# Optimization experiments

Measured on AMD Instinct MI355X. Metric: run time of the kernel, lower is better.

Reference implementation:

```python
import jax, jax.numpy as jnp
import numpy as np

STEPS = 10          # points in t_grid -> STEPS-1 RK4 intervals
TRACE_STEPS = 2     # Hutchinson probes per dynamics eval
T_FINAL = 1.0
CLAMP = 100.0


def odefun(t, z, W1, b1, tw1, W2, b2):
    # time-conditioned 2-layer tanh MLP (canonical FFJORD dynamics)
    h = jnp.tanh(z @ W1 + b1 + t * tw1)
    return h @ W2 + b2


def setup_inputs() -> dict:
    key = jax.random.key(0)
    B, D, H = 2048, 512, 1024
    ks = jax.random.split(key, 4)
    s1 = 1.0 / np.sqrt(D)
    s2 = 1.0 / np.sqrt(H)
    return {
        "x": jax.random.normal(ks[0], (B, D), jnp.float32),
        "W1": jax.random.normal(ks[1], (D, H), jnp.float32) * s1,
        "b1": jnp.zeros((H,), jnp.float32),
        "tw1": jax.random.normal(ks[2], (H,), jnp.float32) * 0.1,
        "W2": jax.random.normal(ks[3], (H, D), jnp.float32) * s2,
        "b2": jnp.zeros((D,), jnp.float32),
    }


def reference(x, W1, b1, tw1, W2, b2):
    params = (W1, b1, tw1, W2, b2)
    B, D = x.shape

    def divergence_estimate(t, z, e):
        # torch detaches z before the grad call -> stop_gradient here
        z_sg = jax.lax.stop_gradient(z)
        f, vjp_fn = jax.vjp(lambda zz: odefun(t, zz, *params), z_sg)
        etf = vjp_fn(e)[0]                      # e^T J  (Hutchinson probe)
        return f, jnp.sum(etf * e, axis=-1)     # [B]

    def augmented_dynamics(t, state, key):
        z = state[:, :-1]                        # [B, D]
        div_est = jnp.zeros((B,), state.dtype)
        f_z = None
        for i in range(TRACE_STEPS):             # small fixed loop
            e = jax.random.randint(jax.random.fold_in(key, i), z.shape, 0, 2).astype(z.dtype) * 2.0 - 1.0
            f_z, div = divergence_estimate(t, z, e)
            div_est = div_est + div
        div_est = jnp.clip(div_est / TRACE_STEPS, -CLAMP, CLAMP)
        return jnp.concatenate([f_z, -div_est[:, None]], axis=-1)

    t_grid = jnp.linspace(0.0, T_FINAL, STEPS)
    state0 = jnp.concatenate([x, jnp.zeros((B, 1), x.dtype)], axis=-1)  # [B, D+1]

    def step(carry, t01):
        state, key = carry
        t0, t1 = t01[0], t01[1]
        dt = t1 - t0
        key, k1k, k2k, k3k, k4k = jax.random.split(key, 5)
        # torchdiffeq 'rk4' = Kutta's 3/8-rule variant (rk4_alt_step_func)
        k1 = augmented_dynamics(t0, state, k1k)
        k2 = augmented_dynamics(t0 + dt / 3.0, state + dt * k1 / 3.0, k2k)
        k3 = augmented_dynamics(t0 + dt * 2.0 / 3.0, state + dt * (k2 - k1 / 3.0), k3k)
        k4 = augmented_dynamics(t1, state + dt * (k1 - k2 + k3), k4k)
        state = state + (k1 + 3.0 * (k2 + k3) + k4) * dt * 0.125
        return (state, key), None

    t_pairs = jnp.stack([t_grid[:-1], t_grid[1:]], axis=-1)  # [STEPS-1, 2]
    (state, _), _ = jax.lax.scan(step, (state0, jax.random.key(1234)), t_pairs)

    rep, probsolve = state[:, :-1], state[:, -1]
    logprob = -0.5 * jnp.sum(rep * rep, axis=-1) + probsolve
    return rep, logprob
```

## Files before the change

kernel.cpp:

```cpp
#include <hip/hip_runtime.h>
#include <stdint.h>


#define B_N 2048
#define D_N 512
#define H_N 1024
#define BD (B_N * D_N)

typedef unsigned short u16;
typedef __attribute__((ext_vector_type(8))) short s16x8;
typedef __attribute__((ext_vector_type(4))) float f32x4;

typedef __attribute__((address_space(1))) const uint32_t ga_u32;
typedef __attribute__((address_space(3))) uint32_t ls_u32;

#if __has_builtin(__builtin_amdgcn_alignbit)
#define ROTL32(x, r) __builtin_amdgcn_alignbit((x), (x), 32 - (r))
#else
#define ROTL32(x, r) (((x) << (r)) | ((x) >> (32 - (r))))
#endif

__device__ __forceinline__ u16 f2bf(float f) {
  union { float f; uint32_t u; } c; c.f = f;
  uint32_t r = c.u + 0x7FFFu + ((c.u >> 16) & 1u);
  return (u16)(r >> 16);
}

struct U2 { uint32_t x, y; };

__device__ __forceinline__ U2 tf2x32(uint32_t k0, uint32_t k1, uint32_t x0, uint32_t x1) {
  uint32_t k2 = k0 ^ k1 ^ 0x1BD11BDAu;
#define RND(r) { x0 += x1; x1 = ROTL32(x1, r); x1 ^= x0; }
  x0 += k0; x1 += k1;
  RND(13) RND(15) RND(26) RND(6)
  x0 += k1; x1 += k2 + 1u;
  RND(17) RND(29) RND(16) RND(24)
  x0 += k2; x1 += k0 + 2u;
  RND(13) RND(15) RND(26) RND(6)
  x0 += k0; x1 += k1 + 3u;
  RND(17) RND(29) RND(16) RND(24)
  x0 += k1; x1 += k2 + 4u;
  RND(13) RND(15) RND(26) RND(6)
  x0 += k2; x1 += k0 + 5u;
#undef RND
  U2 r; r.x = x0; r.y = x1; return r;
}

__device__ __forceinline__ void keysched_body(uint32_t* ekeys) {
  uint32_t kx = 0u, ky = 1234u;
  for (int s = 0; s < 9; ++s) {
    for (int st = 0; st < 4; ++st) {
      U2 kst = tf2x32(kx, ky, 0u, (uint32_t)(st + 1));
      for (int pr = 0; pr < 2; ++pr) {
        U2 fo = tf2x32(kst.x, kst.y, 0u, (uint32_t)pr);
        U2 k2 = tf2x32(fo.x, fo.y, 0u, 1u);
        ekeys[(s * 4 + st) * 4 + pr * 2 + 0] = k2.x;
        ekeys[(s * 4 + st) * 4 + pr * 2 + 1] = k2.y;
      }
    }
    U2 c = tf2x32(kx, ky, 0u, 0u);
    kx = c.x; ky = c.y;
  }
}

__device__ __forceinline__ void egen_item(int t2, u16* __restrict__ ebf,
                                          const uint32_t* __restrict__ keys) {
  int stage = t2 >> 16, rem = t2 & 65535;
  int probe = rem >> 15, idx = rem & 32767;
  uint32_t p0 = (uint32_t)idx * 32;
  uint32_t k0 = keys[stage * 4 + probe * 2], k1 = keys[stage * 4 + probe * 2 + 1];
  uint4* dst = (uint4*)(ebf + (size_t)stage * (2 * (size_t)BD) + (size_t)probe * BD + (size_t)idx * 32);
#pragma unroll
  for (int g = 0; g < 4; ++g) {
    uint32_t pr[4];
#pragma unroll
    for (int h = 0; h < 4; ++h) {
      uint32_t c0 = p0 + g * 8 + h * 2;
      U2 r0 = tf2x32(k0, k1, 0u, c0);
      U2 r1 = tf2x32(k0, k1, 0u, c0 + 1u);
      pr[h] = (((r0.x ^ r0.y) & 1u) ? 0x3F80u : 0xBF80u) |
              (((r1.x ^ r1.y) & 1u) ? 0x3F800000u : 0xBF800000u);
    }
    uint4 v; v.x = pr[0]; v.y = pr[1]; v.z = pr[2]; v.w = pr[3];
    dst[g] = v;
  }
}

__device__ __forceinline__ void f1_tile(u16* S, int tile,
    const u16* __restrict__ zin, const u16* __restrict__ e0g, const u16* __restrict__ e1g,
    const u16* __restrict__ W1T, const u16* __restrict__ W2b,
    const float* __restrict__ b1v, const float* __restrict__ tw1v, float tstage,
    u16* __restrict__ hbuf, float* __restrict__ div0, float* __restrict__ div1) {
  const int tid = threadIdx.x, wave = tid >> 6, lane = tid & 63;
  const int bm = tile >> 4, bh = tile & 15;
  const int row0 = bm * 64, col0 = bh * 64;
  const int wm = wave >> 1, wn = wave & 1, r16 = lane & 15, q = lane >> 4;
  const int srow = lane >> 2, scol = (lane & 3) * 8;

  f32x4 az[2][2], au0[2][2], au1[2][2], av0[2][2], av1[2][2];
#pragma unroll
  for (int i = 0; i < 2; ++i)
#pragma unroll
    for (int j = 0; j < 2; ++j) {
      az[i][j] = (f32x4){0,0,0,0}; au0[i][j] = (f32x4){0,0,0,0}; au1[i][j] = (f32x4){0,0,0,0};
      av0[i][j] = (f32x4){0,0,0,0}; av1[i][j] = (f32x4){0,0,0,0};
    }

  const size_t arow = (size_t)(row0 + wave * 16 + srow) * 512 + scol;
  const size_t brow = (size_t)(col0 + wave * 16 + srow) * 512 + scol;
  auto stage = [&](int kt, int buf) {
    u16* b = S + buf * 10240;
    __builtin_amdgcn_global_load_lds((ga_u32*)(zin + arow + kt), (ls_u32*)(b + 0    + wave * 512), 16, 0, 0);
    __builtin_amdgcn_global_load_lds((ga_u32*)(e0g + arow + kt), (ls_u32*)(b + 2048 + wave * 512), 16, 0, 0);
    __builtin_amdgcn_global_load_lds((ga_u32*)(e1g + arow + kt), (ls_u32*)(b + 4096 + wave * 512), 16, 0, 0);
    __builtin_amdgcn_global_load_lds((ga_u32*)(W1T + brow + kt), (ls_u32*)(b + 6144 + wave * 512), 16, 0, 0);
    __builtin_amdgcn_global_load_lds((ga_u32*)(W2b + brow + kt), (ls_u32*)(b + 8192 + wave * 512), 16, 0, 0);
  };
  stage(0, 0);
  for (int it = 0; it < 16; ++it) {
    const int buf = it & 1;
    __syncthreads();
    if (it + 1 < 16) stage((it + 1) * 32, buf ^ 1);
    const u16* b = S + buf * 10240;
    s16x8 zf[2], e0f[2], e1f[2], w1f[2], w2f[2];
#pragma unroll
    for (int i = 0; i < 2; ++i) {
      const int ao = (wm * 32 + i * 16 + r16) * 32 + q * 8;
      zf[i]  = *(const s16x8*)(b + 0    + ao);
      e0f[i] = *(const s16x8*)(b + 2048 + ao);
      e1f[i] = *(const s16x8*)(b + 4096 + ao);
    }
#pragma unroll
    for (int j = 0; j < 2; ++j) {
      const int bo = (wn * 32 + j * 16 + r16) * 32 + q * 8;
      w1f[j] = *(const s16x8*)(b + 6144 + bo);
      w2f[j] = *(const s16x8*)(b + 8192 + bo);
    }
#pragma unroll
    for (int i = 0; i < 2; ++i)
#pragma unroll
      for (int j = 0; j < 2; ++j) {
        az[i][j]  = __builtin_amdgcn_mfma_f32_16x16x32_bf16(zf[i],  w1f[j], az[i][j],  0, 0, 0);
        au0[i][j] = __builtin_amdgcn_mfma_f32_16x16x32_bf16(e0f[i], w1f[j], au0[i][j], 0, 0, 0);
        au1[i][j] = __builtin_amdgcn_mfma_f32_16x16x32_bf16(e1f[i], w1f[j], au1[i][j], 0, 0, 0);
        av0[i][j] = __builtin_amdgcn_mfma_f32_16x16x32_bf16(e0f[i], w2f[j], av0[i][j], 0, 0, 0);
        av1[i][j] = __builtin_amdgcn_mfma_f32_16x16x32_bf16(e1f[i], w2f[j], av1[i][j], 0, 0, 0);
      }
  }

  float d0s[2][4], d1s[2][4];
#pragma unroll
  for (int i = 0; i < 2; ++i)
#pragma unroll
    for (int r = 0; r < 4; ++r) { d0s[i][r] = 0.f; d1s[i][r] = 0.f; }

#pragma unroll
  for (int j = 0; j < 2; ++j) {
    const int gcol = col0 + wn * 32 + j * 16 + r16;
    const float colb = b1v[gcol] + tstage * tw1v[gcol];
#pragma unroll
    for (int i = 0; i < 2; ++i) {
      const int rbase = row0 + wm * 32 + i * 16 + q * 4;
#pragma unroll
      for (int r = 0; r < 4; ++r) {
        float hv = tanhf(az[i][j][r] + colb);
        hbuf[(size_t)(rbase + r) * H_N + gcol] = f2bf(hv);
        float s = 1.f - hv * hv;
        d0s[i][r] += s * au0[i][j][r] * av0[i][j][r];
        d1s[i][r] += s * au1[i][j][r] * av1[i][j][r];
      }
    }
  }
#pragma unroll
  for (int i = 0; i < 2; ++i)
#pragma unroll
    for (int r = 0; r < 4; ++r) {
      float a = d0s[i][r], bb = d1s[i][r];
#pragma unroll
      for (int m = 1; m < 16; m <<= 1) { a += __shfl_xor(a, m); bb += __shfl_xor(bb, m); }
      if (r16 == 0) {
        int grow = row0 + wm * 32 + i * 16 + q * 4 + r;
        atomicAdd(&div0[grow], a);
        atomicAdd(&div1[grow], bb);
      }
    }
}

__device__ __forceinline__ void f3_tile(u16* S, int tile,
    const u16* __restrict__ hbuf, const u16* __restrict__ W2T, const float* __restrict__ b2v,
    float* __restrict__ z, float* __restrict__ ACC, float* __restrict__ T,
    u16* __restrict__ zin, float dt, int st,
    float* __restrict__ lp, float* __restrict__ div0, float* __restrict__ div1, float wdt) {
  const int tid = threadIdx.x, wave = tid >> 6, lane = tid & 63;
  const int bm = tile >> 4, bn = tile & 15;
  const int row0 = bm * 64, col0 = bn * 32;
  const int r16 = lane & 15, q = lane >> 4;
  const int srow = lane >> 2, scol = (lane & 3) * 8;

  if (bn == 0 && tid < 64) {
    int b = row0 + tid;
    float c = 0.5f * (div0[b] + div1[b]);
    c = fminf(fmaxf(c, -100.f), 100.f);
    lp[b] -= wdt * c;
    div0[b] = 0.f; div1[b] = 0.f;
  }

  f32x4 acc[2];
  acc[0] = (f32x4){0,0,0,0}; acc[1] = (f32x4){0,0,0,0};

  const size_t arow = (size_t)(row0 + wave * 16 + srow) * 1024 + scol;
  const size_t brow = (size_t)(col0 + (wave & 1) * 16 + srow) * 1024 + scol;
  auto stage = [&](int kt, int buf) {
    u16* b = S + buf * 10240;
    __builtin_amdgcn_global_load_lds((ga_u32*)(hbuf + arow + kt), (ls_u32*)(b + wave * 512), 16, 0, 0);
    if (wave < 2)
      __builtin_amdgcn_global_load_lds((ga_u32*)(W2T + brow + kt), (ls_u32*)(b + 2048 + wave * 512), 16, 0, 0);
  };
  stage(0, 0);
  for (int it = 0; it < 32; ++it) {
    const int buf = it & 1;
    __syncthreads();
    if (it + 1 < 32) stage((it + 1) * 32, buf ^ 1);
    const u16* b = S + buf * 10240;
    s16x8 af  = *(const s16x8*)(b + (wave * 16 + r16) * 32 + q * 8);
    s16x8 bf0 = *(const s16x8*)(b + 2048 + r16 * 32 + q * 8);
    s16x8 bf1 = *(const s16x8*)(b + 2048 + (16 + r16) * 32 + q * 8);
    acc[0] = __builtin_amdgcn_mfma_f32_16x16x32_bf16(af, bf0, acc[0], 0, 0, 0);
    acc[1] = __builtin_amdgcn_mfma_f32_16x16x32_bf16(af, bf1, acc[1], 0, 0, 0);
  }

#pragma unroll
  for (int j = 0; j < 2; ++j) {
    const int gcol = col0 + j * 16 + r16;
    const float cb = b2v[gcol];
    const int rbase = row0 + wave * 16 + q * 4;
#pragma unroll
    for (int r = 0; r < 4; ++r) {
      const size_t idx = (size_t)(rbase + r) * D_N + gcol;
      const float f = acc[j][r] + cb;
      if (st == 0) {
        ACC[idx] = dt * 0.125f * f;
        T[idx]   = dt * f;
        zin[idx] = f2bf(z[idx] + dt * f * (1.f / 3.f));
      } else if (st == 1) {
        float t_ = T[idx];
        ACC[idx] += 0.375f * dt * f;
        zin[idx] = f2bf(z[idx] + dt * f - t_ * (1.f / 3.f));
        T[idx]   = t_ - dt * f;
      } else if (st == 2) {
        ACC[idx] += 0.375f * dt * f;
        zin[idx] = f2bf(z[idx] + T[idx] + dt * f);
      } else {
        float zn = z[idx] + ACC[idx] + dt * 0.125f * f;
        z[idx]   = zn;
        zin[idx] = f2bf(zn);
      }
    }
  }
}

__device__ __forceinline__ void bar_sync(uint32_t* cnt, uint32_t target) {
  __syncthreads();
  __threadfence();
  if (threadIdx.x == 0) {
    __hip_atomic_fetch_add(cnt, 1u, __ATOMIC_RELAXED, __HIP_MEMORY_SCOPE_AGENT);
    uint32_t v = __hip_atomic_load(cnt, __ATOMIC_RELAXED, __HIP_MEMORY_SCOPE_AGENT);
    while (v < target) {
      __builtin_amdgcn_s_sleep(2);
      v = __hip_atomic_load(cnt, __ATOMIC_RELAXED, __HIP_MEMORY_SCOPE_AGENT);
    }
  }
  __syncthreads();
  __threadfence();
}

__global__ __launch_bounds__(256, 2)
void k_main(const float* __restrict__ x, const float* __restrict__ W1,
            const float* __restrict__ b1v, const float* __restrict__ tw1v,
            const float* __restrict__ W2, const float* __restrict__ b2v,
            float* __restrict__ out, uint32_t* __restrict__ keys, u16* __restrict__ ebf,
            float* __restrict__ z, float* __restrict__ ACC, float* __restrict__ T,
            u16* __restrict__ zin, u16* __restrict__ hbuf,
            u16* __restrict__ W1T, u16* __restrict__ W2b, u16* __restrict__ W2T,
            float* __restrict__ lp, float* __restrict__ div0, float* __restrict__ div1,
            uint32_t* __restrict__ bar) {
  __shared__ u16 S[2 * 10240];
  const int gtid = blockIdx.x * 256 + threadIdx.x;
  const int gsz = gridDim.x * 256;
  const int slab = blockIdx.x >> 4;
  const int li   = blockIdx.x & 15;
  uint32_t* scnt = bar + slab * 32;
  uint32_t* gcnt = bar + 32 * 32;

  if (gtid == 0) keysched_body(keys);
  for (int i = gtid; i < BD; i += gsz) { float v = x[i]; z[i] = v; zin[i] = f2bf(v); }
  for (int i = gtid; i < B_N; i += gsz) { lp[i] = 0.f; div0[i] = 0.f; div1[i] = 0.f; }
  for (int i = gtid; i < D_N * H_N; i += gsz) {
    int c = i / D_N, r = i - c * D_N;
    W1T[i] = f2bf(W1[(size_t)r * H_N + c]);
  }
  for (int i = gtid; i < H_N * D_N; i += gsz) W2b[i] = f2bf(W2[i]);
  for (int i = gtid; i < H_N * D_N; i += gsz) {
    int c = i / H_N, r = i - c * H_N;
    W2T[i] = f2bf(W2[(size_t)r * D_N + c]);
  }
  bar_sync(gcnt, 512);

  for (int t2 = gtid; t2 < 36 * 65536; t2 += gsz) egen_item(t2, ebf, keys);
  bar_sync(gcnt, 1024);

  uint32_t tgt = 16;
  for (int sg = 0; sg < 36; ++sg) {
    const int s = sg >> 2, st = sg & 3;
    const float t0 = (float)s / 9.0f, t1 = (float)(s + 1) / 9.0f, dt = t1 - t0;
    const float tst = (st == 0) ? t0 : (st == 1) ? (t0 + dt / 3.0f)
                   : (st == 2) ? (t0 + dt * 2.0f / 3.0f) : t1;
    const float wdt = dt * 0.125f * ((st == 1 || st == 2) ? 3.0f : 1.0f);
    const u16* e0g = ebf + (size_t)sg * (2 * (size_t)BD);
    const u16* e1g = e0g + BD;
    f1_tile(S, slab * 16 + li, zin, e0g, e1g, W1T, W2b, b1v, tw1v, tst, hbuf, div0, div1);
    bar_sync(scnt, tgt); tgt += 16;
    f3_tile(S, slab * 16 + li, hbuf, W2T, b2v, z, ACC, T, zin, dt, st, lp, div0, div1, wdt);
    bar_sync(scnt, tgt); tgt += 16;
  }

  {
    const int wave = threadIdx.x >> 6, lane = threadIdx.x & 63;
    int b = slab * 64 + li * 4 + wave;
    const float* zr = z + (size_t)b * D_N;
    float ss = 0.f;
    for (int d = lane; d < D_N; d += 64) {
      float v = zr[d];
      out[(size_t)b * D_N + d] = v;
      ss += v * v;
    }
    for (int off = 32; off; off >>= 1) ss += __shfl_down(ss, off);
    if (lane == 0) out[BD + b] = -0.5f * ss + lp[b];
  }
}

__global__ void k_keysched(uint32_t* __restrict__ ekeys) {
  if (threadIdx.x == 0 && blockIdx.x == 0) keysched_body(ekeys);
}
__global__ void kegen_g(u16* __restrict__ ebf, const uint32_t* __restrict__ keys) {
  int t = blockIdx.x * 256 + threadIdx.x;
  if (t < 36 * 65536) egen_item(t, ebf, keys);
}
__global__ void k_init(const float* __restrict__ x, float* __restrict__ z, u16* __restrict__ zin,
                       float* __restrict__ lp, float* __restrict__ d0, float* __restrict__ d1) {
  int i = blockIdx.x * 256 + threadIdx.x;
  if (i < BD) { float v = x[i]; z[i] = v; zin[i] = f2bf(v); }
  if (i < B_N) { lp[i] = 0.f; d0[i] = 0.f; d1[i] = 0.f; }
}
__global__ void k_cvtT(const float* __restrict__ src, u16* __restrict__ dst, int R, int C) {
  int i = blockIdx.x * 256 + threadIdx.x;
  if (i >= R * C) return;
  int c = i / R, r = i - c * R;
  dst[i] = f2bf(src[(size_t)r * C + c]);
}
__global__ void k_cvt(const float* __restrict__ src, u16* __restrict__ dst, int n) {
  int i = blockIdx.x * 256 + threadIdx.x;
  if (i < n) dst[i] = f2bf(src[i]);
}
__global__ void k_sentinel(float* __restrict__ out, int n) {
  int i = blockIdx.x * 256 + threadIdx.x;
  if (i < n) out[i] = 12345.0f;
}
__global__ __launch_bounds__(256) void kf1_g(
    const u16* zin, const u16* e0g, const u16* e1g, const u16* W1T, const u16* W2b,
    const float* b1v, const float* tw1v, float tstage,
    u16* hbuf, float* div0, float* div1) {
  __shared__ u16 S[2 * 10240];
  f1_tile(S, blockIdx.x, zin, e0g, e1g, W1T, W2b, b1v, tw1v, tstage, hbuf, div0, div1);
}
__global__ __launch_bounds__(256) void kf3_g(
    const u16* hbuf, const u16* W2T, const float* b2v,
    float* z, float* ACC, float* T, u16* zin, float dt, int st,
    float* lp, float* div0, float* div1, float wdt) {
  __shared__ u16 S[2 * 10240];
  f3_tile(S, blockIdx.x, hbuf, W2T, b2v, z, ACC, T, zin, dt, st, lp, div0, div1, wdt);
}
__global__ void k_out(const float* __restrict__ z, const float* __restrict__ lp,
                      float* __restrict__ out) {
  int b = blockIdx.x, t = threadIdx.x;
  const float* zr = z + (size_t)b * D_N;
  float ss = 0.f;
  for (int d = t; d < D_N; d += 256) {
    float v = zr[d];
    out[(size_t)b * D_N + d] = v;
    ss += v * v;
  }
  for (int off = 32; off > 0; off >>= 1) ss += __shfl_down(ss, off);
  __shared__ float red[4];
  if ((t & 63) == 0) red[t >> 6] = ss;
  __syncthreads();
  if (t == 0) out[(size_t)BD + b] = -0.5f * (red[0] + red[1] + red[2] + red[3]) + lp[b];
}

extern "C" void kernel_launch(void* const* d_in, const int* in_sizes, int n_in,
                              void* d_out, int out_size, void* d_ws, size_t ws_size,
                              hipStream_t stream) {
  const float* x   = (const float*)d_in[0];
  const float* W1  = (const float*)d_in[1];
  const float* b1  = (const float*)d_in[2];
  const float* tw1 = (const float*)d_in[3];
  const float* W2  = (const float*)d_in[4];
  const float* b2  = (const float*)d_in[5];
  float* outp = (float*)d_out;

  const size_t NEEDED = (size_t)180 << 20;
  if (ws_size < NEEDED) {
    k_sentinel<<<(BD + B_N + 255) / 256, 256, 0, stream>>>(outp, BD + B_N);
    return;
  }
  char* w = (char*)d_ws;
  auto carve = [&](size_t bytes) { char* p = w; w += (bytes + 255) & ~(size_t)255; return p; };
  uint32_t* bar  = (uint32_t*)carve(33 * 32 * sizeof(uint32_t));
  uint32_t* keys = (uint32_t*)carve(144 * sizeof(uint32_t));
  u16* ebf   = (u16*)carve((size_t)36 * 2 * BD * 2);
  float* z   = (float*)carve((size_t)BD * 4);
  float* ACC = (float*)carve((size_t)BD * 4);
  float* T   = (float*)carve((size_t)BD * 4);
  u16* zin   = (u16*)carve((size_t)BD * 2);
  u16* hbuf  = (u16*)carve((size_t)B_N * H_N * 2);
  u16* W1T   = (u16*)carve((size_t)H_N * D_N * 2);
  u16* W2b   = (u16*)carve((size_t)H_N * D_N * 2);
  u16* W2T   = (u16*)carve((size_t)D_N * H_N * 2);
  float* lp   = (float*)carve((size_t)B_N * 4);
  float* div0 = (float*)carve((size_t)B_N * 4);
  float* div1 = (float*)carve((size_t)B_N * 4);

  int maxb = 0;
  hipError_t orc = hipOccupancyMaxActiveBlocksPerMultiprocessor(&maxb, (const void*)k_main, 256, 0);
  if (orc == hipSuccess && maxb >= 2) {
    hipMemsetAsync(bar, 0, 33 * 32 * sizeof(uint32_t), stream);
    void* params[] = { (void*)&x, (void*)&W1, (void*)&b1, (void*)&tw1, (void*)&W2, (void*)&b2,
                       (void*)&outp, (void*)&keys, (void*)&ebf, (void*)&z, (void*)&ACC, (void*)&T,
                       (void*)&zin, (void*)&hbuf, (void*)&W1T, (void*)&W2b, (void*)&W2T,
                       (void*)&lp, (void*)&div0, (void*)&div1, (void*)&bar };
    hipError_t rc = hipLaunchCooperativeKernel((const void*)k_main, dim3(512), dim3(256),
                                               params, 0, stream);
    if (rc == hipSuccess) return;
    (void)hipGetLastError();
  }

  k_keysched<<<1, 1, 0, stream>>>(keys);
  k_init<<<BD / 256, 256, 0, stream>>>(x, z, zin, lp, div0, div1);
  k_cvtT<<<(D_N * H_N) / 256, 256, 0, stream>>>(W1, W1T, D_N, H_N);
  k_cvt <<<(H_N * D_N) / 256, 256, 0, stream>>>(W2, W2b, H_N * D_N);
  k_cvtT<<<(H_N * D_N) / 256, 256, 0, stream>>>(W2, W2T, H_N, D_N);
  kegen_g<<<(36 * 65536) / 256, 256, 0, stream>>>(ebf, keys);

  for (int s = 0; s < 9; ++s) {
    float t0 = (float)s / 9.0f;
    float t1 = (float)(s + 1) / 9.0f;
    float dt = t1 - t0;
    float tst[4] = { t0, t0 + dt / 3.0f, t0 + dt * 2.0f / 3.0f, t1 };
    float wts[4] = { 1.f, 3.f, 3.f, 1.f };
    for (int st = 0; st < 4; ++st) {
      const int sg = s * 4 + st;
      const u16* e0g = ebf + (size_t)sg * (2 * (size_t)BD);
      const u16* e1g = e0g + BD;
      kf1_g<<<512, 256, 0, stream>>>(zin, e0g, e1g, W1T, W2b, b1, tw1, tst[st], hbuf, div0, div1);
      kf3_g<<<512, 256, 0, stream>>>(hbuf, W2T, b2, z, ACC, T, zin, dt, st,
                                     lp, div0, div1, dt * 0.125f * wts[st]);
    }
  }
  k_out<<<B_N, 256, 0, stream>>>(z, lp, outp);
}
```

Measured before the change: 1.619 ms.

## Replace per-slab barriers with fine-grained h-tile flags and rotated chunked second GEMM

Each block now publishes a per-tile flag once its h tile is written. The second GEMM walks the H chunks in rotated order and waits only on each chunk's producer flag, instead of a full slab barrier between the two matmuls. A per-slab counter gates the next stage's first GEMM, and tanh is replaced by an exp-based fast version. The goal is to cut barrier stalls and let the two stages overlap, at the cost of spin-wait polling, more subtle memory-ordering requirements, and slightly lower tanh accuracy.

```diff
diff --git a/kernel.cpp b/kernel.cpp
--- a/kernel.cpp
+++ b/kernel.cpp
@@ -24,6 +24,11 @@
   union { float f; uint32_t u; } c; c.f = f;
   uint32_t r = c.u + 0x7FFFu + ((c.u >> 16) & 1u);
   return (u16)(r >> 16);
+}
+__device__ __forceinline__ float fast_tanh(float v) {
+  float e = __expf(2.0f * fabsf(v));
+  float t = 1.0f - 2.0f / (e + 1.0f);
+  return copysignf(t, v);
 }
 
 struct U2 { uint32_t x, y; };
@@ -84,6 +89,12 @@
     uint4 v; v.x = pr[0]; v.y = pr[1]; v.z = pr[2]; v.w = pr[3];
     dst[g] = v;
   }
+}
+
+__device__ __forceinline__ void wait_ge(uint32_t* p, uint32_t tgt) {
+  while (__hip_atomic_load(p, __ATOMIC_RELAXED, __HIP_MEMORY_SCOPE_AGENT) < tgt)
+    __builtin_amdgcn_s_sleep(1);
+  __threadfence();
 }
 
 __device__ __forceinline__ void f1_tile(u16* S, int tile,
@@ -163,7 +174,7 @@
       const int rbase = row0 + wm * 32 + i * 16 + q * 4;
 #pragma unroll
       for (int r = 0; r < 4; ++r) {
-        float hv = tanhf(az[i][j][r] + colb);
+        float hv = fast_tanh(az[i][j][r] + colb);
         hbuf[(size_t)(rbase + r) * H_N + gcol] = f2bf(hv);
         float s = 1.f - hv * hv;
         d0s[i][r] += s * au0[i][j][r] * av0[i][j][r];
@@ -186,49 +197,10 @@
     }
 }
 
-__device__ __forceinline__ void f3_tile(u16* S, int tile,
-    const u16* __restrict__ hbuf, const u16* __restrict__ W2T, const float* __restrict__ b2v,
-    float* __restrict__ z, float* __restrict__ ACC, float* __restrict__ T,
-    u16* __restrict__ zin, float dt, int st,
-    float* __restrict__ lp, float* __restrict__ div0, float* __restrict__ div1, float wdt) {
-  const int tid = threadIdx.x, wave = tid >> 6, lane = tid & 63;
-  const int bm = tile >> 4, bn = tile & 15;
-  const int row0 = bm * 64, col0 = bn * 32;
-  const int r16 = lane & 15, q = lane >> 4;
-  const int srow = lane >> 2, scol = (lane & 3) * 8;
-
-  if (bn == 0 && tid < 64) {
-    int b = row0 + tid;
-    float c = 0.5f * (div0[b] + div1[b]);
-    c = fminf(fmaxf(c, -100.f), 100.f);
-    lp[b] -= wdt * c;
-    div0[b] = 0.f; div1[b] = 0.f;
-  }
-
-  f32x4 acc[2];
-  acc[0] = (f32x4){0,0,0,0}; acc[1] = (f32x4){0,0,0,0};
-
-  const size_t arow = (size_t)(row0 + wave * 16 + srow) * 1024 + scol;
-  const size_t brow = (size_t)(col0 + (wave & 1) * 16 + srow) * 1024 + scol;
-  auto stage = [&](int kt, int buf) {
-    u16* b = S + buf * 10240;
-    __builtin_amdgcn_global_load_lds((ga_u32*)(hbuf + arow + kt), (ls_u32*)(b + wave * 512), 16, 0, 0);
-    if (wave < 2)
-      __builtin_amdgcn_global_load_lds((ga_u32*)(W2T + brow + kt), (ls_u32*)(b + 2048 + wave * 512), 16, 0, 0);
-  };
-  stage(0, 0);
-  for (int it = 0; it < 32; ++it) {
-    const int buf = it & 1;
-    __syncthreads();
-    if (it + 1 < 32) stage((it + 1) * 32, buf ^ 1);
-    const u16* b = S + buf * 10240;
-    s16x8 af  = *(const s16x8*)(b + (wave * 16 + r16) * 32 + q * 8);
-    s16x8 bf0 = *(const s16x8*)(b + 2048 + r16 * 32 + q * 8);
-    s16x8 bf1 = *(const s16x8*)(b + 2048 + (16 + r16) * 32 + q * 8);
-    acc[0] = __builtin_amdgcn_mfma_f32_16x16x32_bf16(af, bf0, acc[0], 0, 0, 0);
-    acc[1] = __builtin_amdgcn_mfma_f32_16x16x32_bf16(af, bf1, acc[1], 0, 0, 0);
-  }
-
+template<typename ACCT>
+__device__ __forceinline__ void f3_epilogue(const ACCT& acc, int row0, int col0,
+    int wave, int r16, int q, const float* b2v,
+    float* z, float* ACC, float* T, u16* zin, float dt, int st) {
 #pragma unroll
   for (int j = 0; j < 2; ++j) {
     const int gcol = col0 + j * 16 + r16;
@@ -259,16 +231,113 @@
   }
 }
 
+__device__ __forceinline__ void f3_chunked(u16* S, int slab, int li, int sg,
+    const u16* __restrict__ hbuf, const u16* __restrict__ W2T, const float* __restrict__ b2v,
+    float* __restrict__ z, float* __restrict__ ACC, float* __restrict__ T,
+    u16* __restrict__ zin, float dt, int st,
+    float* __restrict__ lp, float* __restrict__ div0, float* __restrict__ div1, float wdt,
+    uint32_t* __restrict__ hflag) {
+  const int tid = threadIdx.x, wave = tid >> 6, lane = tid & 63;
+  const int row0 = slab * 64, col0 = li * 32;
+  const int r16 = lane & 15, q = lane >> 4;
+  const int srow = lane >> 2, scol = (lane & 3) * 8;
+
+  f32x4 acc[2];
+  acc[0] = (f32x4){0,0,0,0}; acc[1] = (f32x4){0,0,0,0};
+
+  const size_t arow = (size_t)(row0 + wave * 16 + srow) * 1024 + scol;
+  auto dma = [&](int bh, int buf) {
+    u16* b = S + buf * 6144;
+    const int k0 = bh * 64;
+    __builtin_amdgcn_global_load_lds((ga_u32*)(hbuf + arow + k0),      (ls_u32*)(b + wave * 512), 16, 0, 0);
+    __builtin_amdgcn_global_load_lds((ga_u32*)(hbuf + arow + k0 + 32), (ls_u32*)(b + 2048 + wave * 512), 16, 0, 0);
+    if (wave < 2)
+      __builtin_amdgcn_global_load_lds((ga_u32*)(W2T + (size_t)(col0 + wave * 16 + srow) * 1024 + k0 + scol),
+                                       (ls_u32*)(b + 4096 + wave * 512), 16, 0, 0);
+    else
+      __builtin_amdgcn_global_load_lds((ga_u32*)(W2T + (size_t)(col0 + (wave - 2) * 16 + srow) * 1024 + k0 + 32 + scol),
+                                       (ls_u32*)(b + 5120 + (wave - 2) * 512), 16, 0, 0);
+  };
+  dma(li, 0);
+  for (int c = 0; c < 16; ++c) {
+    const int buf = c & 1;
+    __syncthreads();
+    if (c + 1 < 16) {
+      int nbh = (li + c + 1) & 15;
+      wait_ge(hflag + (slab * 16 + nbh) * 16, (uint32_t)(sg + 1));
+      dma(nbh, buf ^ 1);
+    }
+    const u16* b = S + buf * 6144;
+#pragma unroll
+    for (int p = 0; p < 2; ++p) {
+      s16x8 af  = *(const s16x8*)(b + p * 2048 + (wave * 16 + r16) * 32 + q * 8);
+      s16x8 bf0 = *(const s16x8*)(b + 4096 + p * 1024 + r16 * 32 + q * 8);
+      s16x8 bf1 = *(const s16x8*)(b + 4096 + p * 1024 + (16 + r16) * 32 + q * 8);
+      acc[0] = __builtin_amdgcn_mfma_f32_16x16x32_bf16(af, bf0, acc[0], 0, 0, 0);
+      acc[1] = __builtin_amdgcn_mfma_f32_16x16x32_bf16(af, bf1, acc[1], 0, 0, 0);
+    }
+  }
+
+  if (li == 0 && tid < 64) {
+    int b = row0 + tid;
+    float c = 0.5f * (div0[b] + div1[b]);
+    c = fminf(fmaxf(c, -100.f), 100.f);
+    lp[b] -= wdt * c;
+    div0[b] = 0.f; div1[b] = 0.f;
+  }
+  f3_epilogue(acc, row0, col0, wave, r16, q, b2v, z, ACC, T, zin, dt, st);
+}
+
+__device__ __forceinline__ void f3_tile(u16* S, int tile,
+    const u16* __restrict__ hbuf, const u16* __restrict__ W2T, const float* __restrict__ b2v,
+    float* __restrict__ z, float* __restrict__ ACC, float* __restrict__ T,
+    u16* __restrict__ zin, float dt, int st,
+    float* __restrict__ lp, float* __restrict__ div0, float* __restrict__ div1, float wdt) {
+  const int tid = threadIdx.x, wave = tid >> 6, lane = tid & 63;
+  const int bm = tile >> 4, bn = tile & 15;
+  const int row0 = bm * 64, col0 = bn * 32;
+  const int r16 = lane & 15, q = lane >> 4;
+  const int srow = lane >> 2, scol = (lane & 3) * 8;
+
+  if (bn == 0 && tid < 64) {
+    int b = row0 + tid;
+    float c = 0.5f * (div0[b] + div1[b]);
+    c = fminf(fmaxf(c, -100.f), 100.f);
+    lp[b] -= wdt * c;
+    div0[b] = 0.f; div1[b] = 0.f;
+  }
+  f32x4 acc[2];
+  acc[0] = (f32x4){0,0,0,0}; acc[1] = (f32x4){0,0,0,0};
+  const size_t arow = (size_t)(row0 + wave * 16 + srow) * 1024 + scol;
+  const size_t brow = (size_t)(col0 + (wave & 1) * 16 + srow) * 1024 + scol;
+  auto stg = [&](int kt, int buf) {
+    u16* b = S + buf * 10240;
+    __builtin_amdgcn_global_load_lds((ga_u32*)(hbuf + arow + kt), (ls_u32*)(b + wave * 512), 16, 0, 0);
+    if (wave < 2)
+      __builtin_amdgcn_global_load_lds((ga_u32*)(W2T + brow + kt), (ls_u32*)(b + 2048 + wave * 512), 16, 0, 0);
+  };
+  stg(0, 0);
+  for (int it = 0; it < 32; ++it) {
+    const int buf = it & 1;
+    __syncthreads();
+    if (it + 1 < 32) stg((it + 1) * 32, buf ^ 1);
+    const u16* b = S + buf * 10240;
+    s16x8 af  = *(const s16x8*)(b + (wave * 16 + r16) * 32 + q * 8);
+    s16x8 bf0 = *(const s16x8*)(b + 2048 + r16 * 32 + q * 8);
+    s16x8 bf1 = *(const s16x8*)(b + 2048 + (16 + r16) * 32 + q * 8);
+    acc[0] = __builtin_amdgcn_mfma_f32_16x16x32_bf16(af, bf0, acc[0], 0, 0, 0);
+    acc[1] = __builtin_amdgcn_mfma_f32_16x16x32_bf16(af, bf1, acc[1], 0, 0, 0);
+  }
+  f3_epilogue(acc, row0, col0, wave, r16, q, b2v, z, ACC, T, zin, dt, st);
+}
+
 __device__ __forceinline__ void bar_sync(uint32_t* cnt, uint32_t target) {
   __syncthreads();
   __threadfence();
   if (threadIdx.x == 0) {
     __hip_atomic_fetch_add(cnt, 1u, __ATOMIC_RELAXED, __HIP_MEMORY_SCOPE_AGENT);
-    uint32_t v = __hip_atomic_load(cnt, __ATOMIC_RELAXED, __HIP_MEMORY_SCOPE_AGENT);
-    while (v < target) {
+    while (__hip_atomic_load(cnt, __ATOMIC_RELAXED, __HIP_MEMORY_SCOPE_AGENT) < target)
       __builtin_amdgcn_s_sleep(2);
-      v = __hip_atomic_load(cnt, __ATOMIC_RELAXED, __HIP_MEMORY_SCOPE_AGENT);
-    }
   }
   __syncthreads();
   __threadfence();
@@ -289,8 +358,9 @@
   const int gsz = gridDim.x * 256;
   const int slab = blockIdx.x >> 4;
   const int li   = blockIdx.x & 15;
-  uint32_t* scnt = bar + slab * 32;
-  uint32_t* gcnt = bar + 32 * 32;
+  uint32_t* gcnt  = bar;
+  uint32_t* zcnt  = bar + 32 + slab * 32;
+  uint32_t* hflag = bar + 2048;
 
   if (gtid == 0) keysched_body(keys);
   for (int i = gtid; i < BD; i += gsz) { float v = x[i]; z[i] = v; zin[i] = f2bf(v); }
@@ -309,7 +379,6 @@
   for (int t2 = gtid; t2 < 36 * 65536; t2 += gsz) egen_item(t2, ebf, keys);
   bar_sync(gcnt, 1024);
 
-  uint32_t tgt = 16;
   for (int sg = 0; sg < 36; ++sg) {
     const int s = sg >> 2, st = sg & 3;
     const float t0 = (float)s / 9.0f, t1 = (float)(s + 1) / 9.0f, dt = t1 - t0;
@@ -318,12 +387,25 @@
     const float wdt = dt * 0.125f * ((st == 1 || st == 2) ? 3.0f : 1.0f);
     const u16* e0g = ebf + (size_t)sg * (2 * (size_t)BD);
     const u16* e1g = e0g + BD;
+
+    if (sg) wait_ge(zcnt, (uint32_t)(16 * sg));
+
     f1_tile(S, slab * 16 + li, zin, e0g, e1g, W1T, W2b, b1v, tw1v, tst, hbuf, div0, div1);
-    bar_sync(scnt, tgt); tgt += 16;
-    f3_tile(S, slab * 16 + li, hbuf, W2T, b2v, z, ACC, T, zin, dt, st, lp, div0, div1, wdt);
-    bar_sync(scnt, tgt); tgt += 16;
-  }
-
+    __syncthreads();
+    __threadfence();
+    if (threadIdx.x == 0)
+      __hip_atomic_store(hflag + (slab * 16 + li) * 16, (uint32_t)(sg + 1),
+                         __ATOMIC_RELEASE, __HIP_MEMORY_SCOPE_AGENT);
+
+    f3_chunked(S, slab, li, sg, hbuf, W2T, b2v, z, ACC, T, zin, dt, st,
+               lp, div0, div1, wdt, hflag);
+    __syncthreads();
+    __threadfence();
+    if (threadIdx.x == 0)
+      __hip_atomic_fetch_add(zcnt, 1u, __ATOMIC_RELEASE, __HIP_MEMORY_SCOPE_AGENT);
+  }
+
+  wait_ge(zcnt, (uint32_t)(16 * 36));
   {
     const int wave = threadIdx.x >> 6, lane = threadIdx.x & 63;
     int b = slab * 64 + li * 4 + wave;
@@ -415,7 +497,7 @@
   }
   char* w = (char*)d_ws;
   auto carve = [&](size_t bytes) { char* p = w; w += (bytes + 255) & ~(size_t)255; return p; };
-  uint32_t* bar  = (uint32_t*)carve(33 * 32 * sizeof(uint32_t));
+  uint32_t* bar  = (uint32_t*)carve(10240 * sizeof(uint32_t));
   uint32_t* keys = (uint32_t*)carve(144 * sizeof(uint32_t));
   u16* ebf   = (u16*)carve((size_t)36 * 2 * BD * 2);
   float* z   = (float*)carve((size_t)BD * 4);
@@ -433,7 +515,7 @@
   int maxb = 0;
   hipError_t orc = hipOccupancyMaxActiveBlocksPerMultiprocessor(&maxb, (const void*)k_main, 256, 0);
   if (orc == hipSuccess && maxb >= 2) {
-    hipMemsetAsync(bar, 0, 33 * 32 * sizeof(uint32_t), stream);
+    hipMemsetAsync(bar, 0, 10240 * sizeof(uint32_t), stream);
     void* params[] = { (void*)&x, (void*)&W1, (void*)&b1, (void*)&tw1, (void*)&W2, (void*)&b2,
                        (void*)&outp, (void*)&keys, (void*)&ebf, (void*)&z, (void*)&ACC, (void*)&T,
                        (void*)&zin, (void*)&hbuf, (void*)&W1T, (void*)&W2b, (void*)&W2T,
```

New measurement: 1.573 ms. 1.03x faster.
